# Kernel optimization log

Measured on AMD Instinct MI355X. Metric: run time of the kernel, lower is better.

Reference implementation:

```python
import jax, jax.numpy as jnp
import numpy as np

MAX_LENGTH = 160
SOS_TOKEN = 0
HIDDEN = 512
EMB = 64
VOCAB = 128
BATCH = 2048


def setup_inputs() -> dict:
    key = jax.random.key(0)
    ks = jax.random.split(key, 10)
    s = 1.0 / np.sqrt(HIDDEN)
    return {
        "encoder_outputs": jax.random.normal(ks[0], (BATCH, 1, HIDDEN), dtype=jnp.float32),
        "encoder_hidden": jax.random.normal(ks[1], (1, BATCH, HIDDEN), dtype=jnp.float32),
        "target_tensor": jax.random.randint(ks[2], (BATCH, MAX_LENGTH), 0, VOCAB),
        "embedding": jax.random.normal(ks[3], (VOCAB, EMB), dtype=jnp.float32),
        "W_ih": jax.random.uniform(ks[4], (3 * HIDDEN, EMB), minval=-s, maxval=s, dtype=jnp.float32),
        "W_hh": jax.random.uniform(ks[5], (3 * HIDDEN, HIDDEN), minval=-s, maxval=s, dtype=jnp.float32),
        "b_ih": jax.random.uniform(ks[6], (3 * HIDDEN,), minval=-s, maxval=s, dtype=jnp.float32),
        "b_hh": jax.random.uniform(ks[7], (3 * HIDDEN,), minval=-s, maxval=s, dtype=jnp.float32),
        "W_out": jax.random.uniform(ks[8], (VOCAB, HIDDEN), minval=-s, maxval=s, dtype=jnp.float32),
        "b_out": jax.random.uniform(ks[9], (VOCAB,), minval=-s, maxval=s, dtype=jnp.float32),
    }


def _decode(encoder_hidden, target_tensor, embedding, W_ih, W_hh, b_ih, b_hh, W_out, b_out):
    B = target_tensor.shape[0]
    # teacher-forced input tokens: [SOS, t0, t1, ..., t_{158}] -> [T, B]
    sos = jnp.full((B, 1), SOS_TOKEN, dtype=target_tensor.dtype)
    tokens = jnp.concatenate([sos, target_tensor[:, : MAX_LENGTH - 1]], axis=1).T
    h0 = encoder_hidden[0]  # [B, H]

    def step(h, tok):
        x = jax.nn.relu(embedding[tok])                    # [B, EMB]
        gi = x @ W_ih.T + b_ih                             # [B, 3H]
        gh = h @ W_hh.T + b_hh                             # [B, 3H]
        i_r, i_z, i_n = jnp.split(gi, 3, axis=-1)
        h_r, h_z, h_n = jnp.split(gh, 3, axis=-1)
        r = jax.nn.sigmoid(i_r + h_r)
        z = jax.nn.sigmoid(i_z + h_z)
        n = jnp.tanh(i_n + r * h_n)
        h_new = (1.0 - z) * n + z * h
        logits = h_new @ W_out.T + b_out                   # [B, V]
        return h_new, logits

    h_last, logits = jax.lax.scan(step, h0, tokens)        # logits: [T, B, V]
    log_probs = jax.nn.log_softmax(logits, axis=-1)        # matches permute(1,0,2) of [B,T,V]
    return log_probs, h_last[None]                          # [T,B,V], [1,B,H]


def reference(encoder_outputs, encoder_hidden, target_tensor, embedding, W_ih, W_hh, b_ih, b_hh, W_out, b_out):
    log_probs, hidden = _decode(encoder_hidden, target_tensor, embedding, W_ih, W_hh, b_ih, b_hh, W_out, b_out)
    return log_probs, hidden
```

## Files before the change

### kernel.cpp

```cpp
#include <hip/hip_runtime.h>
#include <hip/hip_bf16.h>

typedef __bf16 bf16x8 __attribute__((ext_vector_type(8)));
typedef float  f32x4  __attribute__((ext_vector_type(4)));

#define MFMA_BF16(a, b, c) __builtin_amdgcn_mfma_f32_16x16x32_bf16((a), (b), (c), 0, 0, 0)

constexpr int TT = 160, BB = 2048, HH = 512, EE = 64, VV = 128, G3 = 1536;
constexpr size_t LPROB_ELEMS = (size_t)TT * BB * VV;

constexpr int BSTRIDE = 1040;
constexpr int GSZ = 16 * BSTRIDE;
constexpr int SMEM_BYTES = 3 * GSZ;
constexpr int WSTRIDE = 264;
constexpr int LLDS_OFF = 128 * WSTRIDE;

__device__ __forceinline__ float fsigmoid(float x) {
  return 1.0f / (1.0f + __expf(-x));
}
__device__ __forceinline__ float ftanh(float x) {
  float ax = fabsf(x);
  float e = __expf(-2.0f * ax);
  float r = (1.0f - e) / (1.0f + e);
  return x < 0.0f ? -r : r;
}
__device__ __forceinline__ float ld(const void* p, long i, int isbf) {
  return isbf ? (float)((const __bf16*)p)[i] : ((const float*)p)[i];
}

__global__ __launch_bounds__(256) void probe_dtype(
    const unsigned short* __restrict__ eh, int* __restrict__ flagp) {
  __shared__ int sb[256];
  int tid = threadIdx.x;
  int cnt = 0;
  for (int i = tid; i < 4096; i += 256) {
    unsigned short u = eh[i];
    int e = (u >> 7) & 0xFF;
    if ((u & 0x7FFF) == 0 || (e >= 90 && e <= 150)) cnt++;
  }
  sb[tid] = cnt;
  __syncthreads();
  for (int s = 128; s > 0; s >>= 1) {
    if (tid < s) sb[tid] += sb[tid + s];
    __syncthreads();
  }
  if (tid == 0) *flagp = (sb[0] > 3072) ? 1 : 0;
}

__global__ __launch_bounds__(256) void conv_w(
    const void* __restrict__ Whh, const void* __restrict__ Wout,
    const void* __restrict__ bhh, const void* __restrict__ bout,
    const int* __restrict__ flagp,
    __bf16* __restrict__ Whh_b, __bf16* __restrict__ Wout_b,
    float* __restrict__ bhhn_f, float* __restrict__ bout_f) {
  const int isbf = *flagp;
  int idx = blockIdx.x * 256 + threadIdx.x;
  Whh_b[idx] = (__bf16)ld(Whh, idx, isbf);
  if (idx < VV * HH) Wout_b[idx] = (__bf16)ld(Wout, idx, isbf);
  if (idx < HH) bhhn_f[idx] = ld(bhh, 2 * HH + idx, isbf);
  if (idx < VV) bout_f[idx] = ld(bout, idx, isbf);
}

__global__ __launch_bounds__(256) void prep_gi(
    const void* __restrict__ emb, const void* __restrict__ Wih,
    const void* __restrict__ bih, const void* __restrict__ bhh,
    const int* __restrict__ flagp, float* __restrict__ gi) {
  const int isbf = *flagp;
  int idx = blockIdx.x * 256 + threadIdx.x;
  int v = idx / G3;
  int n = idx - v * G3;
  float s = 0.0f;
#pragma unroll 8
  for (int k = 0; k < EE; ++k) {
    float x = ld(emb, v * EE + k, isbf);
    x = x > 0.0f ? x : 0.0f;
    s += x * ld(Wih, (long)n * EE + k, isbf);
  }
  s += ld(bih, n, isbf);
  if (n < 2 * HH) s += ld(bhh, n, isbf);
  gi[idx] = s;
}

__global__ __launch_bounds__(256) void prep_h0(
    const void* __restrict__ ehid, const int* __restrict__ flagp,
    float* __restrict__ hf, __bf16* __restrict__ hb0) {
  const int isbf = *flagp;
  int idx = blockIdx.x * 256 + threadIdx.x;
  float v = ld(ehid, idx, isbf);
  hf[idx] = v;
  hb0[idx] = (__bf16)v;
}

__global__ __launch_bounds__(256, 3) void gru_step(
    const __bf16* __restrict__ Whh, const __bf16* __restrict__ Wout,
    const float* __restrict__ bhhn_f, const float* __restrict__ bout_f,
    const float* __restrict__ gi, const int* __restrict__ tgt,
    const int* __restrict__ flagp,
    const __bf16* __restrict__ hbs,
    __bf16* __restrict__ hbd,
    float* __restrict__ hf,
    void* __restrict__ outp, int t) {
  __shared__ __align__(16) char smem[SMEM_BYTES];

  const int tid = threadIdx.x;
  const int bid = blockIdx.x;
  const int w = tid >> 6;
  const int lane = tid & 63;
  const int q = lane >> 4;
  const int l16 = lane & 15;
  const int isbf = *flagp;
  const f32x4 fzero = {0.0f, 0.0f, 0.0f, 0.0f};

  if (bid < 512) {
    if (t == 160) {
      int base = bid * 2048 + tid * 8;
      const float* src = hf + base;
      if (isbf) {
        bf16x8 v;
#pragma unroll
        for (int i = 0; i < 8; ++i) v[i] = (__bf16)src[i];
        *(bf16x8*)((__bf16*)outp + LPROB_ELEMS + base) = v;
      } else {
        f32x4 v0 = *(const f32x4*)src;
        f32x4 v1 = *(const f32x4*)(src + 4);
        float* dst = (float*)outp + LPROB_ELEMS + base;
        *(f32x4*)dst = v0;
        *(f32x4*)(dst + 4) = v1;
      }
      return;
    }
    const int grp = bid & 15;
    const int colTile = bid >> 4;
    const int mBase = grp * 128 + w * 32;
    const int c = colTile * 16 + l16;
    const float bhhn = bhhn_f[c];

    {
      const char* src0 = (const char*)(Whh + (size_t)(colTile * 16) * HH);
#pragma unroll
      for (int g = 0; g < 3; ++g) {
        const char* sg = src0 + (size_t)g * (HH * HH * 2);
#pragma unroll
        for (int j = 0; j < 4; ++j) {
          int off = (tid + j * 256) * 16;
          bf16x8 v = *(const bf16x8*)(sg + off);
          *(bf16x8*)(smem + g * GSZ + (off >> 10) * BSTRIDE + (off & 1023)) = v;
        }
      }
    }

    int tk[2][4];
    float hold[2][4];
#pragma unroll
    for (int ms = 0; ms < 2; ++ms)
#pragma unroll
      for (int rg = 0; rg < 4; ++rg) {
        int row = mBase + ms * 16 + q * 4 + rg;
        tk[ms][rg] = (t == 0) ? 0 : tgt[row * TT + (t - 1)];
        hold[ms][rg] = hf[(size_t)row * HH + c];
      }
    float gv[2][4][3];
#pragma unroll
    for (int ms = 0; ms < 2; ++ms)
#pragma unroll
      for (int rg = 0; rg < 4; ++rg) {
        const float* gvp = gi + (size_t)tk[ms][rg] * G3 + c;
        gv[ms][rg][0] = gvp[0];
        gv[ms][rg][1] = gvp[HH];
        gv[ms][rg][2] = gvp[2 * HH];
      }
    __syncthreads();

    f32x4 acc[2][3];
#pragma unroll
    for (int ms = 0; ms < 2; ++ms)
#pragma unroll
      for (int gg = 0; gg < 3; ++gg) acc[ms][gg] = fzero;

    const __bf16* aRow0 = hbs + (size_t)(mBase + l16) * HH + q * 8;
    const __bf16* aRow1 = aRow0 + 16 * HH;
    const char* bb = smem + l16 * BSTRIDE + q * 16;

#pragma unroll 8
    for (int k0 = 0; k0 < HH; k0 += 32) {
      bf16x8 a0 = *(const bf16x8*)(aRow0 + k0);
      bf16x8 a1 = *(const bf16x8*)(aRow1 + k0);
#pragma unroll
      for (int gg = 0; gg < 3; ++gg) {
        bf16x8 bf = *(const bf16x8*)(bb + gg * GSZ + k0 * 2);
        acc[0][gg] = MFMA_BF16(a0, bf, acc[0][gg]);
        acc[1][gg] = MFMA_BF16(a1, bf, acc[1][gg]);
      }
    }

#pragma unroll
    for (int ms = 0; ms < 2; ++ms) {
#pragma unroll
      for (int rg = 0; rg < 4; ++rg) {
        int row = mBase + ms * 16 + q * 4 + rg;
        float r_ = fsigmoid(acc[ms][0][rg] + gv[ms][rg][0]);
        float z_ = fsigmoid(acc[ms][1][rg] + gv[ms][rg][1]);
        float n_ = ftanh(gv[ms][rg][2] + r_ * (acc[ms][2][rg] + bhhn));
        size_t hi = (size_t)row * HH + c;
        float hv = (1.0f - z_) * n_ + z_ * hold[ms][rg];
        hf[hi] = hv;
        hbd[hi] = (__bf16)hv;
      }
    }
  } else {
    if (t == 0) return;
    const int rb = (bid - 512) * 16;
    const __bf16* aR = hbs + (size_t)(rb + l16) * HH + q * 8;
    float* llds = (float*)(smem + LLDS_OFF);

    bf16x8 afr[16];
#pragma unroll
    for (int i = 0; i < 16; ++i) afr[i] = *(const bf16x8*)(aR + i * 32);

    f32x4 acc2[2];
    acc2[0] = fzero; acc2[1] = fzero;
#pragma unroll
    for (int kc = 0; kc < 4; ++kc) {
#pragma unroll
      for (int j = 0; j < 8; ++j) {
        int off = (tid + j * 256) * 16;
        int row = off >> 8;
        int inrow = off & 255;
        bf16x8 v = *(const bf16x8*)((const char*)Wout +
                                    (size_t)row * 1024 + kc * 256 + inrow);
        *(bf16x8*)(smem + row * WSTRIDE + inrow) = v;
      }
      __syncthreads();
#pragma unroll
      for (int kl = 0; kl < 128; kl += 32) {
        bf16x8 a = afr[kc * 4 + (kl >> 5)];
        bf16x8 b0 = *(const bf16x8*)(smem + (w * 32 + l16) * WSTRIDE + kl * 2 + q * 16);
        bf16x8 b1 = *(const bf16x8*)(smem + (w * 32 + 16 + l16) * WSTRIDE + kl * 2 + q * 16);
        acc2[0] = MFMA_BF16(a, b0, acc2[0]);
        acc2[1] = MFMA_BF16(a, b1, acc2[1]);
      }
      __syncthreads();
    }

#pragma unroll
    for (int j = 0; j < 2; ++j) {
      int col = (w * 2 + j) * 16 + l16;
      float bo = bout_f[col];
#pragma unroll
      for (int rg = 0; rg < 4; ++rg)
        llds[(q * 4 + rg) * 132 + col] = acc2[j][rg] + bo;
    }
    __syncthreads();
    {
      int row = tid >> 4, seg = tid & 15;
      const float* lr = &llds[row * 132 + seg * 8];
      float x[8];
      float m = -3.0e38f;
#pragma unroll
      for (int i = 0; i < 8; ++i) { x[i] = lr[i]; m = fmaxf(m, x[i]); }
#pragma unroll
      for (int d = 1; d < 16; d <<= 1) m = fmaxf(m, __shfl_xor(m, d, 16));
      float s = 0.0f;
#pragma unroll
      for (int i = 0; i < 8; ++i) s += __expf(x[i] - m);
#pragma unroll
      for (int d = 1; d < 16; d <<= 1) s += __shfl_xor(s, d, 16);
      float lg = m + __logf(s);
      size_t ofs = (size_t)(t - 1) * (BB * VV) + (size_t)(rb + row) * VV + seg * 8;
      if (isbf) {
        bf16x8 ov;
#pragma unroll
        for (int i = 0; i < 8; ++i) ov[i] = (__bf16)(x[i] - lg);
        *(bf16x8*)((__bf16*)outp + ofs) = ov;
      } else {
        f32x4 o0, o1;
#pragma unroll
        for (int i = 0; i < 4; ++i) { o0[i] = x[i] - lg; o1[i] = x[4 + i] - lg; }
        float* dst = (float*)outp + ofs;
        *(f32x4*)dst = o0;
        *(f32x4*)(dst + 4) = o1;
      }
    }
  }
}

extern "C" void kernel_launch(void* const* d_in, const int* in_sizes, int n_in,
                              void* d_out, int out_size, void* d_ws, size_t ws_size,
                              hipStream_t stream) {
  const void* ehid = d_in[1];
  const int*  tgt  = (const int*)d_in[2];
  const void* emb  = d_in[3];
  const void* Wih  = d_in[4];
  const void* Whh  = d_in[5];
  const void* bih  = d_in[6];
  const void* bhh  = d_in[7];
  const void* Wout = d_in[8];
  const void* bout = d_in[9];

  char* ws = (char*)d_ws;
  int*    flagp  = (int*)(ws + 0);
  float*  gi     = (float*)(ws + 256);
  float*  hf     = (float*)(ws + 786688);
  __bf16* hb0    = (__bf16*)(ws + 4980992);
  __bf16* hb1    = (__bf16*)(ws + 7078144);
  __bf16* Whh_b  = (__bf16*)(ws + 9175296);
  __bf16* Wout_b = (__bf16*)(ws + 10748160);
  float*  bhhn_f = (float*)(ws + 10879232);
  float*  bout_f = (float*)(ws + 10881280);

  probe_dtype<<<1, 256, 0, stream>>>((const unsigned short*)ehid, flagp);
  conv_w<<<3072, 256, 0, stream>>>(Whh, Wout, bhh, bout, flagp,
                                   Whh_b, Wout_b, bhhn_f, bout_f);
  prep_gi<<<768, 256, 0, stream>>>(emb, Wih, bih, bhh, flagp, gi);
  prep_h0<<<4096, 256, 0, stream>>>(ehid, flagp, hf, hb0);

  for (int t = 0; t <= TT; ++t) {
    const __bf16* hbs = (t & 1) ? hb1 : hb0;
    __bf16*       hbd = (t & 1) ? hb0 : hb1;
    gru_step<<<640, 256, 0, stream>>>(Whh_b, Wout_b, bhhn_f, bout_f, gi, tgt,
                                      flagp, hbs, hbd, hf, d_out, t);
  }
}
```

Measured before the change: 2.855 ms.

## Load W_out fragments directly from global, fold final hidden write into last step

The output-projection blocks no longer stage W_out through LDS in four chunks with barriers. Each wave now reads its B fragments straight from global memory, which removes the eight __syncthreads and the LDS copies in exchange for uncached global reads per wave. The final-hidden copy, previously a separate t==160 pass, is now written inside the t==159 GRU update. Token loads are also hoisted ahead of the W_hh LDS staging so their latency can overlap it.

Result: slower. 3.249 ms (+13.8%).

```diff
diff --git a/kernel.cpp b/kernel.cpp
--- a/kernel.cpp
+++ b/kernel.cpp
@@ -12,8 +12,6 @@
 constexpr int BSTRIDE = 1040;
 constexpr int GSZ = 16 * BSTRIDE;
 constexpr int SMEM_BYTES = 3 * GSZ;
-constexpr int WSTRIDE = 264;
-constexpr int LLDS_OFF = 128 * WSTRIDE;
 
 __device__ __forceinline__ float fsigmoid(float x) {
   return 1.0f / (1.0f + __expf(-x));
@@ -112,29 +110,22 @@
   const f32x4 fzero = {0.0f, 0.0f, 0.0f, 0.0f};
 
   if (bid < 512) {
-    if (t == 160) {
-      int base = bid * 2048 + tid * 8;
-      const float* src = hf + base;
-      if (isbf) {
-        bf16x8 v;
-#pragma unroll
-        for (int i = 0; i < 8; ++i) v[i] = (__bf16)src[i];
-        *(bf16x8*)((__bf16*)outp + LPROB_ELEMS + base) = v;
-      } else {
-        f32x4 v0 = *(const f32x4*)src;
-        f32x4 v1 = *(const f32x4*)(src + 4);
-        float* dst = (float*)outp + LPROB_ELEMS + base;
-        *(f32x4*)dst = v0;
-        *(f32x4*)(dst + 4) = v1;
-      }
-      return;
-    }
+    if (t == 160) return;
     const int grp = bid & 15;
     const int colTile = bid >> 4;
     const int mBase = grp * 128 + w * 32;
     const int c = colTile * 16 + l16;
     const float bhhn = bhhn_f[c];
 
+    int tk[2][4];
+#pragma unroll
+    for (int ms = 0; ms < 2; ++ms)
+#pragma unroll
+      for (int rg = 0; rg < 4; ++rg) {
+        int row = mBase + ms * 16 + q * 4 + rg;
+        tk[ms][rg] = (t == 0) ? 0 : tgt[row * TT + (t - 1)];
+      }
+
     {
       const char* src0 = (const char*)(Whh + (size_t)(colTile * 16) * HH);
 #pragma unroll
@@ -149,14 +140,12 @@
       }
     }
 
-    int tk[2][4];
     float hold[2][4];
 #pragma unroll
     for (int ms = 0; ms < 2; ++ms)
 #pragma unroll
       for (int rg = 0; rg < 4; ++rg) {
         int row = mBase + ms * 16 + q * 4 + rg;
-        tk[ms][rg] = (t == 0) ? 0 : tgt[row * TT + (t - 1)];
         hold[ms][rg] = hf[(size_t)row * HH + c];
       }
     float gv[2][4][3];
@@ -205,41 +194,30 @@
         float hv = (1.0f - z_) * n_ + z_ * hold[ms][rg];
         hf[hi] = hv;
         hbd[hi] = (__bf16)hv;
+        if (t == 159) {
+          size_t o = LPROB_ELEMS + hi;
+          if (isbf) ((__bf16*)outp)[o] = (__bf16)hv;
+          else      ((float*)outp)[o] = hv;
+        }
       }
     }
   } else {
     if (t == 0) return;
     const int rb = (bid - 512) * 16;
-    const __bf16* aR = hbs + (size_t)(rb + l16) * HH + q * 8;
-    float* llds = (float*)(smem + LLDS_OFF);
-
-    bf16x8 afr[16];
-#pragma unroll
-    for (int i = 0; i < 16; ++i) afr[i] = *(const bf16x8*)(aR + i * 32);
+    const __bf16* aR  = hbs + (size_t)(rb + l16) * HH + q * 8;
+    const __bf16* bR0 = Wout + (size_t)(w * 32 + l16) * HH + q * 8;
+    const __bf16* bR1 = bR0 + 16 * HH;
+    float* llds = (float*)smem;
 
     f32x4 acc2[2];
     acc2[0] = fzero; acc2[1] = fzero;
 #pragma unroll
-    for (int kc = 0; kc < 4; ++kc) {
-#pragma unroll
-      for (int j = 0; j < 8; ++j) {
-        int off = (tid + j * 256) * 16;
-        int row = off >> 8;
-        int inrow = off & 255;
-        bf16x8 v = *(const bf16x8*)((const char*)Wout +
-                                    (size_t)row * 1024 + kc * 256 + inrow);
-        *(bf16x8*)(smem + row * WSTRIDE + inrow) = v;
-      }
-      __syncthreads();
-#pragma unroll
-      for (int kl = 0; kl < 128; kl += 32) {
-        bf16x8 a = afr[kc * 4 + (kl >> 5)];
-        bf16x8 b0 = *(const bf16x8*)(smem + (w * 32 + l16) * WSTRIDE + kl * 2 + q * 16);
-        bf16x8 b1 = *(const bf16x8*)(smem + (w * 32 + 16 + l16) * WSTRIDE + kl * 2 + q * 16);
-        acc2[0] = MFMA_BF16(a, b0, acc2[0]);
-        acc2[1] = MFMA_BF16(a, b1, acc2[1]);
-      }
-      __syncthreads();
+    for (int k0 = 0; k0 < HH; k0 += 32) {
+      bf16x8 a  = *(const bf16x8*)(aR + k0);
+      bf16x8 b0 = *(const bf16x8*)(bR0 + k0);
+      bf16x8 b1 = *(const bf16x8*)(bR1 + k0);
+      acc2[0] = MFMA_BF16(a, b0, acc2[0]);
+      acc2[1] = MFMA_BF16(a, b1, acc2[1]);
     }
 
 #pragma unroll
```

## Fuse output projection into GRU gate blocks and pipeline log-softmax one step later

Applied to the files above, without the earlier changes.

The output logits GEMM moves into the GRU recurrence blocks. The column tiles 24-31 reuse the already-loaded h fragments and multiply against Wout read directly from global memory, writing raw logits to double-buffered scratch. A lighter block group then computes the log-softmax for the previous step's logits one launch later, which needs one extra launch. This removes the separate Wout LDS staging and the redundant h reloads, and it shrinks the grid. The cost is extra MFMA work and load imbalance on 8 of the 32 column tiles, plus scratch traffic for the logits.

After: 2.860 ms. Within noise of the previous version (+0.2%).

```diff
diff --git a/kernel.cpp b/kernel.cpp
--- a/kernel.cpp
+++ b/kernel.cpp
@@ -12,8 +12,6 @@
 constexpr int BSTRIDE = 1040;
 constexpr int GSZ = 16 * BSTRIDE;
 constexpr int SMEM_BYTES = 3 * GSZ;
-constexpr int WSTRIDE = 264;
-constexpr int LLDS_OFF = 128 * WSTRIDE;
 
 __device__ __forceinline__ float fsigmoid(float x) {
   return 1.0f / (1.0f + __expf(-x));
@@ -99,6 +97,7 @@
     const __bf16* __restrict__ hbs,
     __bf16* __restrict__ hbd,
     float* __restrict__ hf,
+    float* __restrict__ llog0, float* __restrict__ llog1,
     void* __restrict__ outp, int t) {
   __shared__ __align__(16) char smem[SMEM_BYTES];
 
@@ -112,6 +111,16 @@
   const f32x4 fzero = {0.0f, 0.0f, 0.0f, 0.0f};
 
   if (bid < 512) {
+    if (t == 161) return;
+    const int grp = bid & 15;
+    const int colTile = bid >> 4;
+    const int mBase = grp * 128 + w * 32;
+    const bool doLog = (colTile >= 24) && (t >= 1);
+    const int vt = colTile - 24;
+    float* lw = ((t - 1) & 1) ? llog1 : llog0;
+    const __bf16* aRow0 = hbs + (size_t)(mBase + l16) * HH + q * 8;
+    const __bf16* aRow1 = aRow0 + 16 * HH;
+
     if (t == 160) {
       int base = bid * 2048 + tid * 8;
       const float* src = hf + base;
@@ -127,11 +136,29 @@
         *(f32x4*)dst = v0;
         *(f32x4*)(dst + 4) = v1;
       }
+      if (doLog) {
+        const __bf16* bpo = Wout + (size_t)(vt * 16 + l16) * HH + q * 8;
+        f32x4 acc2[2];
+        acc2[0] = fzero; acc2[1] = fzero;
+#pragma unroll
+        for (int k0 = 0; k0 < HH; k0 += 32) {
+          bf16x8 a0 = *(const bf16x8*)(aRow0 + k0);
+          bf16x8 a1 = *(const bf16x8*)(aRow1 + k0);
+          bf16x8 b  = *(const bf16x8*)(bpo + k0);
+          acc2[0] = MFMA_BF16(a0, b, acc2[0]);
+          acc2[1] = MFMA_BF16(a1, b, acc2[1]);
+        }
+        const float bo = bout_f[vt * 16 + l16];
+#pragma unroll
+        for (int ms = 0; ms < 2; ++ms)
+#pragma unroll
+          for (int rg = 0; rg < 4; ++rg)
+            lw[(size_t)(mBase + ms * 16 + q * 4 + rg) * VV + vt * 16 + l16] =
+                acc2[ms][rg] + bo;
+      }
       return;
     }
-    const int grp = bid & 15;
-    const int colTile = bid >> 4;
-    const int mBase = grp * 128 + w * 32;
+
     const int c = colTile * 16 + l16;
     const float bhhn = bhhn_f[c];
 
@@ -176,10 +203,11 @@
     for (int ms = 0; ms < 2; ++ms)
 #pragma unroll
       for (int gg = 0; gg < 3; ++gg) acc[ms][gg] = fzero;
-
-    const __bf16* aRow0 = hbs + (size_t)(mBase + l16) * HH + q * 8;
-    const __bf16* aRow1 = aRow0 + 16 * HH;
+    f32x4 acc2[2];
+    acc2[0] = fzero; acc2[1] = fzero;
+
     const char* bb = smem + l16 * BSTRIDE + q * 16;
+    const __bf16* bpo = Wout + (size_t)(vt * 16 + l16) * HH + q * 8;
 
 #pragma unroll 8
     for (int k0 = 0; k0 < HH; k0 += 32) {
@@ -190,6 +218,11 @@
         bf16x8 bf = *(const bf16x8*)(bb + gg * GSZ + k0 * 2);
         acc[0][gg] = MFMA_BF16(a0, bf, acc[0][gg]);
         acc[1][gg] = MFMA_BF16(a1, bf, acc[1][gg]);
+      }
+      if (doLog) {
+        bf16x8 b = *(const bf16x8*)(bpo + k0);
+        acc2[0] = MFMA_BF16(a0, b, acc2[0]);
+        acc2[1] = MFMA_BF16(a1, b, acc2[1]);
       }
     }
 
@@ -207,78 +240,50 @@
         hbd[hi] = (__bf16)hv;
       }
     }
+
+    if (doLog) {
+      const float bo = bout_f[vt * 16 + l16];
+#pragma unroll
+      for (int ms = 0; ms < 2; ++ms)
+#pragma unroll
+        for (int rg = 0; rg < 4; ++rg)
+          lw[(size_t)(mBase + ms * 16 + q * 4 + rg) * VV + vt * 16 + l16] =
+              acc2[ms][rg] + bo;
+    }
   } else {
-    if (t == 0) return;
-    const int rb = (bid - 512) * 16;
-    const __bf16* aR = hbs + (size_t)(rb + l16) * HH + q * 8;
-    float* llds = (float*)(smem + LLDS_OFF);
-
-    bf16x8 afr[16];
-#pragma unroll
-    for (int i = 0; i < 16; ++i) afr[i] = *(const bf16x8*)(aR + i * 32);
-
-    f32x4 acc2[2];
-    acc2[0] = fzero; acc2[1] = fzero;
-#pragma unroll
-    for (int kc = 0; kc < 4; ++kc) {
-#pragma unroll
-      for (int j = 0; j < 8; ++j) {
-        int off = (tid + j * 256) * 16;
-        int row = off >> 8;
-        int inrow = off & 255;
-        bf16x8 v = *(const bf16x8*)((const char*)Wout +
-                                    (size_t)row * 1024 + kc * 256 + inrow);
-        *(bf16x8*)(smem + row * WSTRIDE + inrow) = v;
-      }
-      __syncthreads();
-#pragma unroll
-      for (int kl = 0; kl < 128; kl += 32) {
-        bf16x8 a = afr[kc * 4 + (kl >> 5)];
-        bf16x8 b0 = *(const bf16x8*)(smem + (w * 32 + l16) * WSTRIDE + kl * 2 + q * 16);
-        bf16x8 b1 = *(const bf16x8*)(smem + (w * 32 + 16 + l16) * WSTRIDE + kl * 2 + q * 16);
-        acc2[0] = MFMA_BF16(a, b0, acc2[0]);
-        acc2[1] = MFMA_BF16(a, b1, acc2[1]);
-      }
-      __syncthreads();
-    }
-
-#pragma unroll
-    for (int j = 0; j < 2; ++j) {
-      int col = (w * 2 + j) * 16 + l16;
-      float bo = bout_f[col];
-#pragma unroll
-      for (int rg = 0; rg < 4; ++rg)
-        llds[(q * 4 + rg) * 132 + col] = acc2[j][rg] + bo;
-    }
-    __syncthreads();
-    {
-      int row = tid >> 4, seg = tid & 15;
-      const float* lr = &llds[row * 132 + seg * 8];
-      float x[8];
-      float m = -3.0e38f;
-#pragma unroll
-      for (int i = 0; i < 8; ++i) { x[i] = lr[i]; m = fmaxf(m, x[i]); }
-#pragma unroll
-      for (int d = 1; d < 16; d <<= 1) m = fmaxf(m, __shfl_xor(m, d, 16));
-      float s = 0.0f;
-#pragma unroll
-      for (int i = 0; i < 8; ++i) s += __expf(x[i] - m);
-#pragma unroll
-      for (int d = 1; d < 16; d <<= 1) s += __shfl_xor(s, d, 16);
-      float lg = m + __logf(s);
-      size_t ofs = (size_t)(t - 1) * (BB * VV) + (size_t)(rb + row) * VV + seg * 8;
-      if (isbf) {
-        bf16x8 ov;
-#pragma unroll
-        for (int i = 0; i < 8; ++i) ov[i] = (__bf16)(x[i] - lg);
-        *(bf16x8*)((__bf16*)outp + ofs) = ov;
-      } else {
-        f32x4 o0, o1;
-#pragma unroll
-        for (int i = 0; i < 4; ++i) { o0[i] = x[i] - lg; o1[i] = x[4 + i] - lg; }
-        float* dst = (float*)outp + ofs;
-        *(f32x4*)dst = o0;
-        *(f32x4*)(dst + 4) = o1;
+    if (t < 2) return;
+    const int s = t - 2;
+    const float* lr = (s & 1) ? llog1 : llog0;
+    const int row = (bid - 512) * 32 + (tid >> 3);
+    const int seg = tid & 7;
+    const float* src = lr + (size_t)row * VV + seg * 16;
+    float x[16];
+    float m = -3.0e38f;
+#pragma unroll
+    for (int i = 0; i < 16; ++i) { x[i] = src[i]; m = fmaxf(m, x[i]); }
+#pragma unroll
+    for (int d = 1; d < 8; d <<= 1) m = fmaxf(m, __shfl_xor(m, d, 8));
+    float ssum = 0.0f;
+#pragma unroll
+    for (int i = 0; i < 16; ++i) ssum += __expf(x[i] - m);
+#pragma unroll
+    for (int d = 1; d < 8; d <<= 1) ssum += __shfl_xor(ssum, d, 8);
+    float lg = m + __logf(ssum);
+    size_t ofs = (size_t)s * (BB * VV) + (size_t)row * VV + seg * 16;
+    if (isbf) {
+      bf16x8 o0, o1;
+#pragma unroll
+      for (int i = 0; i < 8; ++i) { o0[i] = (__bf16)(x[i] - lg); o1[i] = (__bf16)(x[8 + i] - lg); }
+      *(bf16x8*)((__bf16*)outp + ofs) = o0;
+      *(bf16x8*)((__bf16*)outp + ofs + 8) = o1;
+    } else {
+      float* dst = (float*)outp + ofs;
+#pragma unroll
+      for (int i = 0; i < 16; i += 4) {
+        f32x4 o;
+#pragma unroll
+        for (int j = 0; j < 4; ++j) o[j] = x[i + j] - lg;
+        *(f32x4*)(dst + i) = o;
       }
     }
   }
@@ -307,6 +312,8 @@
   __bf16* Wout_b = (__bf16*)(ws + 10748160);
   float*  bhhn_f = (float*)(ws + 10879232);
   float*  bout_f = (float*)(ws + 10881280);
+  float*  llog0  = (float*)(ws + 10881792);
+  float*  llog1  = (float*)(ws + 11930368);
 
   probe_dtype<<<1, 256, 0, stream>>>((const unsigned short*)ehid, flagp);
   conv_w<<<3072, 256, 0, stream>>>(Whh, Wout, bhh, bout, flagp,
@@ -314,10 +321,11 @@
   prep_gi<<<768, 256, 0, stream>>>(emb, Wih, bih, bhh, flagp, gi);
   prep_h0<<<4096, 256, 0, stream>>>(ehid, flagp, hf, hb0);
 
-  for (int t = 0; t <= TT; ++t) {
+  for (int t = 0; t <= 161; ++t) {
     const __bf16* hbs = (t & 1) ? hb1 : hb0;
     __bf16*       hbd = (t & 1) ? hb0 : hb1;
-    gru_step<<<640, 256, 0, stream>>>(Whh_b, Wout_b, bhhn_f, bout_f, gi, tgt,
-                                      flagp, hbs, hbd, hf, d_out, t);
-  }
-}
+    gru_step<<<576, 256, 0, stream>>>(Whh_b, Wout_b, bhhn_f, bout_f, gi, tgt,
+                                      flagp, hbs, hbd, hf, llog0, llog1,
+                                      d_out, t);
+  }
+}
```
